# Performance work log

Hardware: AMD Instinct MI355X
Metric: run time of the kernel (lower is better)

The kernel has to match this reference:

```python
import jax, jax.numpy as jnp
import numpy as np

B, S, H = 8, 1024, 1024
NH, HD = 16, 64
LN_EPS = 1e-12


def setup_inputs() -> dict:
    key = jax.random.key(0)
    ks = jax.random.split(key, 8)
    sd = 0.02
    return {
        "hidden_states": jax.random.normal(ks[0], (B, S, H), jnp.float32),
        "attention_mask": jnp.zeros((B, 1, 1, S), jnp.float32),
        "Wq": jax.random.normal(ks[1], (H, H), jnp.float32) * sd,
        "bq": jnp.zeros((H,), jnp.float32),
        "Wk": jax.random.normal(ks[2], (H, H), jnp.float32) * sd,
        "bk": jnp.zeros((H,), jnp.float32),
        "Wv": jax.random.normal(ks[3], (H, H), jnp.float32) * sd,
        "bv": jnp.zeros((H,), jnp.float32),
        "Wo": jax.random.normal(ks[4], (H, H), jnp.float32) * sd,
        "bo": jnp.zeros((H,), jnp.float32),
        "ln_gamma": jnp.ones((H,), jnp.float32),
        "ln_beta": jnp.zeros((H,), jnp.float32),
    }


def _heads(x):
    # [B,S,H] -> [B,NH,S,HD]
    return x.reshape(B, S, NH, HD).transpose(0, 2, 1, 3)


def reference(hidden_states, attention_mask, Wq, bq, Wk, bk, Wv, bv, Wo, bo, ln_gamma, ln_beta):
    # QKV projections (torch Linear: x @ W.T + b)
    q = _heads(hidden_states @ Wq.T + bq)
    k = _heads(hidden_states @ Wk.T + bk)
    v = _heads(hidden_states @ Wv.T + bv)
    # scaled dot-product attention with additive mask
    scores = jnp.einsum("bhqd,bhkd->bhqk", q, k) / np.sqrt(HD).astype(np.float32)
    scores = scores + attention_mask  # broadcast [B,1,1,S]
    probs = jax.nn.softmax(scores, axis=-1)
    ctx = jnp.einsum("bhqk,bhkd->bhqd", probs, v)
    ctx = ctx.transpose(0, 2, 1, 3).reshape(B, S, H)
    # output projection + residual + LayerNorm
    out = ctx @ Wo.T + bo
    x = out + hidden_states
    mu = jnp.mean(x, axis=-1, keepdims=True)
    var = jnp.var(x, axis=-1, keepdims=True)
    return (x - mu) * jax.lax.rsqrt(var + LN_EPS) * ln_gamma + ln_beta
```

## Files before the change

kernel.cpp:

```cpp
#include <hip/hip_runtime.h>
#include <stdint.h>

typedef __attribute__((ext_vector_type(8))) __bf16 bf16x8;
typedef __attribute__((ext_vector_type(8))) unsigned short ushortx8;
typedef __attribute__((ext_vector_type(4))) unsigned short ushortx4;
typedef __attribute__((ext_vector_type(4))) short short4v;
typedef __attribute__((ext_vector_type(4))) float floatx4;

#define ASYNC16(g, l) __builtin_amdgcn_global_load_lds( \
    (__attribute__((address_space(1))) void*)(g),       \
    (__attribute__((address_space(3))) void*)(l), 16, 0, 0)

__device__ __forceinline__ unsigned short f2bf(float f) {
    unsigned int u = __float_as_uint(f);
    u += 0x7fffu + ((u >> 16) & 1u);
    return (unsigned short)(u >> 16);
}

__device__ __forceinline__ floatx4 mfma32(bf16x8 a, bf16x8 b, floatx4 c) {
    return __builtin_amdgcn_mfma_f32_16x16x32_bf16(a, b, c, 0, 0, 0);
}
__device__ __forceinline__ floatx4 mfma16(short4v a, short4v b, floatx4 c) {
    return __builtin_amdgcn_mfma_f32_16x16x16bf16_1k(a, b, c, 0, 0, 0);
}

__global__ __launch_bounds__(256) void cvt_bf16(const float* __restrict__ in,
                                                unsigned short* __restrict__ out,
                                                int n8) {
    int i = blockIdx.x * 256 + threadIdx.x;
    if (i >= n8) return;
    const float4* p = (const float4*)in + (size_t)i * 2;
    float4 a = p[0], b = p[1];
    ushortx8 o;
    o[0] = f2bf(a.x); o[1] = f2bf(a.y); o[2] = f2bf(a.z); o[3] = f2bf(a.w);
    o[4] = f2bf(b.x); o[5] = f2bf(b.y); o[6] = f2bf(b.z); o[7] = f2bf(b.w);
    *((ushortx8*)out + i) = o;
}

__global__ __launch_bounds__(256) void gemm_qkv(
    const unsigned short* __restrict__ A,
    const unsigned short* __restrict__ W,
    const float* __restrict__ bq, const float* __restrict__ bk, const float* __restrict__ bv,
    unsigned short* __restrict__ Qo, unsigned short* __restrict__ Ko, unsigned short* __restrict__ Vo)
{
    __shared__ unsigned short As[128 * 32];
    __shared__ unsigned short Bs[128 * 32];
    const int K = 1024;
    const int t = threadIdx.x;
    const int wave = t >> 6, lane = t & 63;
    const int quad = lane >> 4, l16 = lane & 15;
    const int wm = (wave >> 1) * 64, wn = (wave & 1) * 64;

    const unsigned short* Ag = A + (size_t)blockIdx.x * 128 * K + (t >> 2) * K + (t & 3) * 8;
    const unsigned short* Wg = W + (size_t)blockIdx.y * 128 * K + (t >> 2) * K + (t & 3) * 8;

    floatx4 acc[4][4] = {};

    for (int k0 = 0; k0 < K; k0 += 32) {
        __syncthreads();
        ASYNC16(Ag + k0,          As + t * 8);
        ASYNC16(Ag + 64 * K + k0, As + 2048 + t * 8);
        ASYNC16(Wg + k0,          Bs + t * 8);
        ASYNC16(Wg + 64 * K + k0, Bs + 2048 + t * 8);
        __syncthreads();
        bf16x8 af[4], bfr[4];
#pragma unroll
        for (int mt = 0; mt < 4; mt++)
            af[mt] = *(const bf16x8*)(As + (wm + mt * 16 + l16) * 32 + quad * 8);
#pragma unroll
        for (int nt = 0; nt < 4; nt++)
            bfr[nt] = *(const bf16x8*)(Bs + (wn + nt * 16 + l16) * 32 + quad * 8);
#pragma unroll
        for (int mt = 0; mt < 4; mt++)
#pragma unroll
            for (int nt = 0; nt < 4; nt++)
                acc[mt][nt] = mfma32(af[mt], bfr[nt], acc[mt][nt]);
    }

    int mat = (blockIdx.y * 128) >> 10;
    if (mat == 2) {
#pragma unroll
        for (int nt = 0; nt < 4; nt++) {
            int feat = (blockIdx.y * 128 + wn + nt * 16 + l16) & 1023;
            float bias = bv[feat];
            int h = feat >> 6, d = feat & 63;
#pragma unroll
            for (int mt = 0; mt < 4; mt++) {
                int sg = blockIdx.x * 128 + wm + mt * 16 + quad * 4;
                int b = sg >> 10, s = sg & 1023;
                ushortx4 o4;
#pragma unroll
                for (int r = 0; r < 4; r++) o4[r] = f2bf(acc[mt][nt][r] + bias);
                *(ushortx4*)(Vo + (((size_t)(b * 16 + h) * 64 + d) * 1024 + s)) = o4;
            }
        }
    } else {
        const float* bp = (mat == 0) ? bq : bk;
        unsigned short* op = (mat == 0) ? Qo : Ko;
#pragma unroll
        for (int nt = 0; nt < 4; nt++) {
            int feat = (blockIdx.y * 128 + wn + nt * 16 + l16) & 1023;
            float bias = bp[feat];
            int h = feat >> 6, d = feat & 63;
#pragma unroll
            for (int mt = 0; mt < 4; mt++) {
#pragma unroll
                for (int r = 0; r < 4; r++) {
                    int gm = blockIdx.x * 128 + wm + mt * 16 + quad * 4 + r;
                    int b = gm >> 10, s = gm & 1023;
                    op[(((size_t)b * 16 + h) * 1024 + s) * 64 + d] = f2bf(acc[mt][nt][r] + bias);
                }
            }
        }
    }
}

__global__ __launch_bounds__(256) void attn(
    const unsigned short* __restrict__ Q,
    const unsigned short* __restrict__ Kg,
    const unsigned short* __restrict__ Vt,
    const float* __restrict__ mask,
    unsigned short* __restrict__ ctx)
{
    __shared__ unsigned short Qs[64 * 64];
    __shared__ unsigned short Ks[64 * 64];
    __shared__ unsigned short Vs[64 * 64];
    __shared__ float Msall[1024];

    const int t = threadIdx.x;
    const int wave = t >> 6, lane = t & 63, quad = lane >> 4, l16 = lane & 15;
    const int s7 = l16 & 7;
    const int head = blockIdx.y;
    const int b = head >> 4, h = head & 15;
    const int q0 = blockIdx.x * 64;
    const unsigned short* Qh = Q + (size_t)head * 65536;
    const unsigned short* Kh = Kg + (size_t)head * 65536;
    const unsigned short* Vh = Vt + (size_t)head * 65536;

    *(float4*)(Msall + t * 4) = *(const float4*)(mask + b * 1024 + t * 4);

    {
        int row = t >> 3, cg = (t & 7) ^ (row & 7);
        ASYNC16(Qh + (size_t)(q0 + row) * 64 + cg * 8, Qs + t * 8);
        ASYNC16(Qh + (size_t)(q0 + row + 32) * 64 + cg * 8, Qs + 2048 + t * 8);
    }
    __syncthreads();
    int qrow = wave * 16 + l16;
    bf16x8 qf0 = *(const bf16x8*)(Qs + qrow * 64 + ((quad ^ s7) * 8));
    bf16x8 qf1 = *(const bf16x8*)(Qs + qrow * 64 + (((quad + 4) ^ s7) * 8));

    float rs_acc = 0.f;
    floatx4 o_acc[4] = {};

    for (int k0 = 0; k0 < 1024; k0 += 64) {
        __syncthreads();
        {
            int row = t >> 3, cg = (t & 7) ^ (row & 7);
            ASYNC16(Kh + (size_t)(k0 + row) * 64 + cg * 8, Ks + t * 8);
            ASYNC16(Kh + (size_t)(k0 + row + 32) * 64 + cg * 8, Ks + 2048 + t * 8);
            ASYNC16(Vh + (size_t)row * 1024 + k0 + cg * 8, Vs + t * 8);
            ASYNC16(Vh + (size_t)(row + 32) * 1024 + k0 + cg * 8, Vs + 2048 + t * 8);
        }
        __syncthreads();

        floatx4 st[4];
#pragma unroll
        for (int nt = 0; nt < 4; nt++) {
            int krow = nt * 16 + l16;
            bf16x8 kf0 = *(const bf16x8*)(Ks + krow * 64 + ((quad ^ s7) * 8));
            bf16x8 kf1 = *(const bf16x8*)(Ks + krow * 64 + (((quad + 4) ^ s7) * 8));
            floatx4 z = {0.f, 0.f, 0.f, 0.f};
            z = mfma32(kf0, qf0, z);
            st[nt] = mfma32(kf1, qf1, z);
        }

        short4v pf[4];
#pragma unroll
        for (int nt = 0; nt < 4; nt++) {
            floatx4 mk = *(const floatx4*)(Msall + k0 + nt * 16 + quad * 4);
#pragma unroll
            for (int r = 0; r < 4; r++) {
                float p = __expf(st[nt][r] * 0.125f + mk[r]);
                rs_acc += p;
                pf[nt][r] = (short)(__float_as_uint(p) >> 16);
            }
        }

#pragma unroll
        for (int dt = 0; dt < 4; dt++) {
            int vrow = dt * 16 + l16;
#pragma unroll
            for (int nt = 0; nt < 4; nt++) {
                short4v vf = *(const short4v*)(Vs + vrow * 64 +
                                (((2 * nt + (quad >> 1)) ^ s7) * 8) + (quad & 1) * 4);
                o_acc[dt] = mfma16(vf, pf[nt], o_acc[dt]);
            }
        }
    }

    rs_acc += __shfl_xor(rs_acc, 16);
    rs_acc += __shfl_xor(rs_acc, 32);
    float inv_l = 1.0f / rs_acc;

    int qg = q0 + wave * 16 + l16;
#pragma unroll
    for (int dt = 0; dt < 4; dt++) {
        ushortx4 o4;
#pragma unroll
        for (int r = 0; r < 4; r++) o4[r] = f2bf(o_acc[dt][r] * inv_l);
        *(ushortx4*)(ctx + ((size_t)(b * 1024 + qg)) * 1024 + h * 64 + dt * 16 + quad * 4) = o4;
    }
}

__global__ __launch_bounds__(256) void gemm_proj(
    const unsigned short* __restrict__ A,
    const unsigned short* __restrict__ W,
    const float* __restrict__ bo,
    const float* __restrict__ resid,
    float* __restrict__ X)
{
    __shared__ unsigned short As[128 * 32];
    __shared__ unsigned short Bs[128 * 32];
    const int K = 1024;
    const int t = threadIdx.x;
    const int wave = t >> 6, lane = t & 63;
    const int quad = lane >> 4, l16 = lane & 15;
    const int wm = (wave >> 1) * 64, wn = (wave & 1) * 64;

    const unsigned short* Ag = A + (size_t)blockIdx.x * 128 * K + (t >> 2) * K + (t & 3) * 8;
    const unsigned short* Wg = W + (size_t)blockIdx.y * 128 * K + (t >> 2) * K + (t & 3) * 8;

    floatx4 acc[4][4] = {};

    for (int k0 = 0; k0 < K; k0 += 32) {
        __syncthreads();
        ASYNC16(Ag + k0,          As + t * 8);
        ASYNC16(Ag + 64 * K + k0, As + 2048 + t * 8);
        ASYNC16(Wg + k0,          Bs + t * 8);
        ASYNC16(Wg + 64 * K + k0, Bs + 2048 + t * 8);
        __syncthreads();
        bf16x8 af[4], bfr[4];
#pragma unroll
        for (int mt = 0; mt < 4; mt++)
            af[mt] = *(const bf16x8*)(As + (wm + mt * 16 + l16) * 32 + quad * 8);
#pragma unroll
        for (int nt = 0; nt < 4; nt++)
            bfr[nt] = *(const bf16x8*)(Bs + (wn + nt * 16 + l16) * 32 + quad * 8);
#pragma unroll
        for (int mt = 0; mt < 4; mt++)
#pragma unroll
            for (int nt = 0; nt < 4; nt++)
                acc[mt][nt] = mfma32(af[mt], bfr[nt], acc[mt][nt]);
    }

#pragma unroll
    for (int nt = 0; nt < 4; nt++) {
        int gn = blockIdx.y * 128 + wn + nt * 16 + l16;
        float bias = bo[gn];
#pragma unroll
        for (int mt = 0; mt < 4; mt++) {
#pragma unroll
            for (int r = 0; r < 4; r++) {
                int gm = blockIdx.x * 128 + wm + mt * 16 + quad * 4 + r;
                size_t off = (size_t)gm * 1024 + gn;
                X[off] = acc[mt][nt][r] + bias + resid[off];
            }
        }
    }
}

__global__ __launch_bounds__(256) void ln_k(const float* __restrict__ X,
                                            const float* __restrict__ g,
                                            const float* __restrict__ be,
                                            float* __restrict__ out)
{
    int row = blockIdx.x;
    int t = threadIdx.x;
    const float* xr = X + (size_t)row * 1024;
    float4 v = *(const float4*)(xr + t * 4);
    float s = v.x + v.y + v.z + v.w;
    float ss = v.x * v.x + v.y * v.y + v.z * v.z + v.w * v.w;
    for (int off = 1; off < 64; off <<= 1) {
        s += __shfl_xor(s, off);
        ss += __shfl_xor(ss, off);
    }
    __shared__ float red[8];
    int wave = t >> 6, lane = t & 63;
    if (lane == 0) { red[wave] = s; red[4 + wave] = ss; }
    __syncthreads();
    s = red[0] + red[1] + red[2] + red[3];
    ss = red[4] + red[5] + red[6] + red[7];
    float mu = s * (1.f / 1024.f);
    float var = ss * (1.f / 1024.f) - mu * mu;
    float inv = rsqrtf(var + 1e-12f);
    float4 gv = *(const float4*)(g + t * 4);
    float4 bv = *(const float4*)(be + t * 4);
    float4 o;
    o.x = (v.x - mu) * inv * gv.x + bv.x;
    o.y = (v.y - mu) * inv * gv.y + bv.y;
    o.z = (v.z - mu) * inv * gv.z + bv.z;
    o.w = (v.w - mu) * inv * gv.w + bv.w;
    *(float4*)(out + (size_t)row * 1024 + t * 4) = o;
}

extern "C" void kernel_launch(void* const* d_in, const int* in_sizes, int n_in,
                              void* d_out, int out_size, void* d_ws, size_t ws_size,
                              hipStream_t stream)
{
    const float* hidden = (const float*)d_in[0];
    const float* mask   = (const float*)d_in[1];
    const float* Wq = (const float*)d_in[2];
    const float* bq = (const float*)d_in[3];
    const float* Wk = (const float*)d_in[4];
    const float* bk = (const float*)d_in[5];
    const float* Wv = (const float*)d_in[6];
    const float* bv = (const float*)d_in[7];
    const float* Wo = (const float*)d_in[8];
    const float* bo = (const float*)d_in[9];
    const float* gamma = (const float*)d_in[10];
    const float* beta  = (const float*)d_in[11];
    float* out = (float*)d_out;

    char* ws = (char*)d_ws;
    unsigned short* hid_bf  = (unsigned short*)(ws + 0);
    unsigned short* wqkv_bf = (unsigned short*)(ws + 16777216);
    unsigned short* wo_bf   = (unsigned short*)(ws + 23068672);
    unsigned short* vt_bf   = (unsigned short*)(ws + 25165824);
    unsigned short* ctx_bf  = (unsigned short*)(ws + 41943040);
    unsigned short* q_bf    = (unsigned short*)(ws + 58720256);
    unsigned short* k_bf    = (unsigned short*)(ws + 75497472);
    float* x_f = (float*)(ws + 58720256);

    cvt_bf16<<<4096, 256, 0, stream>>>(hidden, hid_bf, 1048576);
    cvt_bf16<<<512, 256, 0, stream>>>(Wq, wqkv_bf, 131072);
    cvt_bf16<<<512, 256, 0, stream>>>(Wk, wqkv_bf + 1048576, 131072);
    cvt_bf16<<<512, 256, 0, stream>>>(Wv, wqkv_bf + 2097152, 131072);
    cvt_bf16<<<512, 256, 0, stream>>>(Wo, wo_bf, 131072);

    gemm_qkv<<<dim3(64, 24), 256, 0, stream>>>(hid_bf, wqkv_bf, bq, bk, bv, q_bf, k_bf, vt_bf);
    attn<<<dim3(16, 128), 256, 0, stream>>>(q_bf, k_bf, vt_bf, mask, ctx_bf);
    gemm_proj<<<dim3(64, 8), 256, 0, stream>>>(ctx_bf, wo_bf, bo, hidden, x_f);
    ln_k<<<8192, 256, 0, stream>>>(x_f, gamma, beta, out);
}
```

Baseline: 302.1 us.

## Swizzle GEMM LDS tiles, vectorize Q/K stores via swapped MFMA, merge weight casts

Applies an XOR swizzle to the LDS staging column in all GEMMs to cut bank conflicts on fragment reads. It splits the QKV GEMM into separate Q/K and V kernels. The Q/K kernel swaps the MFMA operand order so each lane holds four consecutive features and can write 8-byte vector stores with float4 bias loads, instead of scalar 2-byte scattered stores. It also merges the four weight-conversion launches into one kernel, trading an extra GEMM launch for fewer launches overall.

```diff
diff --git a/kernel.cpp b/kernel.cpp
--- a/kernel.cpp
+++ b/kernel.cpp
@@ -37,25 +37,34 @@
     *((ushortx8*)out + i) = o;
 }
 
-__global__ __launch_bounds__(256) void gemm_qkv(
-    const unsigned short* __restrict__ A,
-    const unsigned short* __restrict__ W,
-    const float* __restrict__ bq, const float* __restrict__ bk, const float* __restrict__ bv,
-    unsigned short* __restrict__ Qo, unsigned short* __restrict__ Ko, unsigned short* __restrict__ Vo)
-{
-    __shared__ unsigned short As[128 * 32];
-    __shared__ unsigned short Bs[128 * 32];
+__global__ __launch_bounds__(256) void cvt_w(const float* __restrict__ Wq,
+                                             const float* __restrict__ Wk,
+                                             const float* __restrict__ Wv,
+                                             const float* __restrict__ Wo,
+                                             unsigned short* __restrict__ oqkv,
+                                             unsigned short* __restrict__ oo) {
+    int blk = blockIdx.x >> 9;
+    const float* src = (blk == 0) ? Wq : (blk == 1) ? Wk : (blk == 2) ? Wv : Wo;
+    unsigned short* dst = (blk == 3) ? oo : oqkv + (size_t)blk * 1048576;
+    int i = (blockIdx.x & 511) * 256 + threadIdx.x;
+    const float4* p = (const float4*)src + (size_t)i * 2;
+    float4 a = p[0], b = p[1];
+    ushortx8 o;
+    o[0] = f2bf(a.x); o[1] = f2bf(a.y); o[2] = f2bf(a.z); o[3] = f2bf(a.w);
+    o[4] = f2bf(b.x); o[5] = f2bf(b.y); o[6] = f2bf(b.z); o[7] = f2bf(b.w);
+    *((ushortx8*)dst + i) = o;
+}
+
+template<bool SWAP>
+__device__ __forceinline__ void kloop_128(
+    const unsigned short* __restrict__ Ag,
+    const unsigned short* __restrict__ Wg,
+    unsigned short* As, unsigned short* Bs,
+    int wm, int wn, int l16, int quad, int t,
+    floatx4 acc[4][4])
+{
     const int K = 1024;
-    const int t = threadIdx.x;
-    const int wave = t >> 6, lane = t & 63;
-    const int quad = lane >> 4, l16 = lane & 15;
-    const int wm = (wave >> 1) * 64, wn = (wave & 1) * 64;
-
-    const unsigned short* Ag = A + (size_t)blockIdx.x * 128 * K + (t >> 2) * K + (t & 3) * 8;
-    const unsigned short* Wg = W + (size_t)blockIdx.y * 128 * K + (t >> 2) * K + (t & 3) * 8;
-
-    floatx4 acc[4][4] = {};
-
+#pragma unroll 1
     for (int k0 = 0; k0 < K; k0 += 32) {
         __syncthreads();
         ASYNC16(Ag + k0,          As + t * 8);
@@ -65,52 +74,109 @@
         __syncthreads();
         bf16x8 af[4], bfr[4];
 #pragma unroll
-        for (int mt = 0; mt < 4; mt++)
-            af[mt] = *(const bf16x8*)(As + (wm + mt * 16 + l16) * 32 + quad * 8);
-#pragma unroll
-        for (int nt = 0; nt < 4; nt++)
-            bfr[nt] = *(const bf16x8*)(Bs + (wn + nt * 16 + l16) * 32 + quad * 8);
-#pragma unroll
-        for (int mt = 0; mt < 4; mt++)
-#pragma unroll
-            for (int nt = 0; nt < 4; nt++)
-                acc[mt][nt] = mfma32(af[mt], bfr[nt], acc[mt][nt]);
-    }
-
-    int mat = (blockIdx.y * 128) >> 10;
-    if (mat == 2) {
+        for (int mt = 0; mt < 4; mt++) {
+            int row = wm + mt * 16 + l16;
+            int p = quad ^ ((row >> 1) & 3);
+            af[mt] = *(const bf16x8*)(As + row * 32 + p * 8);
+        }
 #pragma unroll
         for (int nt = 0; nt < 4; nt++) {
-            int feat = (blockIdx.y * 128 + wn + nt * 16 + l16) & 1023;
-            float bias = bv[feat];
-            int h = feat >> 6, d = feat & 63;
-#pragma unroll
-            for (int mt = 0; mt < 4; mt++) {
-                int sg = blockIdx.x * 128 + wm + mt * 16 + quad * 4;
-                int b = sg >> 10, s = sg & 1023;
-                ushortx4 o4;
-#pragma unroll
-                for (int r = 0; r < 4; r++) o4[r] = f2bf(acc[mt][nt][r] + bias);
-                *(ushortx4*)(Vo + (((size_t)(b * 16 + h) * 64 + d) * 1024 + s)) = o4;
-            }
-        }
-    } else {
-        const float* bp = (mat == 0) ? bq : bk;
-        unsigned short* op = (mat == 0) ? Qo : Ko;
-#pragma unroll
-        for (int nt = 0; nt < 4; nt++) {
-            int feat = (blockIdx.y * 128 + wn + nt * 16 + l16) & 1023;
-            float bias = bp[feat];
-            int h = feat >> 6, d = feat & 63;
-#pragma unroll
-            for (int mt = 0; mt < 4; mt++) {
-#pragma unroll
-                for (int r = 0; r < 4; r++) {
-                    int gm = blockIdx.x * 128 + wm + mt * 16 + quad * 4 + r;
-                    int b = gm >> 10, s = gm & 1023;
-                    op[(((size_t)b * 16 + h) * 1024 + s) * 64 + d] = f2bf(acc[mt][nt][r] + bias);
-                }
-            }
+            int row = wn + nt * 16 + l16;
+            int p = quad ^ ((row >> 1) & 3);
+            bfr[nt] = *(const bf16x8*)(Bs + row * 32 + p * 8);
+        }
+        if (SWAP) {
+#pragma unroll
+            for (int ft = 0; ft < 4; ft++)
+#pragma unroll
+                for (int st = 0; st < 4; st++)
+                    acc[ft][st] = mfma32(bfr[ft], af[st], acc[ft][st]);
+        } else {
+#pragma unroll
+            for (int mt = 0; mt < 4; mt++)
+#pragma unroll
+                for (int nt = 0; nt < 4; nt++)
+                    acc[mt][nt] = mfma32(af[mt], bfr[nt], acc[mt][nt]);
+        }
+    }
+}
+
+__device__ __forceinline__ int stage_col(int t) { return ((t & 3) ^ ((t >> 3) & 3)) * 8; }
+
+__global__ __launch_bounds__(256) void gemm_qk(
+    const unsigned short* __restrict__ A,
+    const unsigned short* __restrict__ W,
+    const float* __restrict__ bq, const float* __restrict__ bk,
+    unsigned short* __restrict__ Qo, unsigned short* __restrict__ Ko)
+{
+    __shared__ unsigned short As[128 * 32];
+    __shared__ unsigned short Bs[128 * 32];
+    const int K = 1024;
+    const int t = threadIdx.x;
+    const int wave = t >> 6, lane = t & 63;
+    const int quad = lane >> 4, l16 = lane & 15;
+    const int wm = (wave >> 1) * 64, wn = (wave & 1) * 64;
+
+    const unsigned short* Ag = A + (size_t)blockIdx.x * 128 * K + (t >> 2) * K + stage_col(t);
+    const unsigned short* Wg = W + (size_t)blockIdx.y * 128 * K + (t >> 2) * K + stage_col(t);
+
+    floatx4 acc[4][4] = {};
+    kloop_128<true>(Ag, Wg, As, Bs, wm, wn, l16, quad, t, acc);
+
+    const float* bp = (blockIdx.y < 8) ? bq : bk;
+    unsigned short* op = (blockIdx.y < 8) ? Qo : Ko;
+#pragma unroll
+    for (int ft = 0; ft < 4; ft++) {
+        int featg = (blockIdx.y * 128 + wn + ft * 16 + quad * 4) & 1023;
+        float4 b4 = *(const float4*)(bp + featg);
+        int h = featg >> 6, d = featg & 63;
+#pragma unroll
+        for (int st = 0; st < 4; st++) {
+            int sg = blockIdx.x * 128 + wm + st * 16 + l16;
+            int b = sg >> 10, s = sg & 1023;
+            ushortx4 o4;
+            o4[0] = f2bf(acc[ft][st][0] + b4.x);
+            o4[1] = f2bf(acc[ft][st][1] + b4.y);
+            o4[2] = f2bf(acc[ft][st][2] + b4.z);
+            o4[3] = f2bf(acc[ft][st][3] + b4.w);
+            *(ushortx4*)(op + (((size_t)(b * 16 + h) * 1024 + s) * 64 + d)) = o4;
+        }
+    }
+}
+
+__global__ __launch_bounds__(256) void gemm_v(
+    const unsigned short* __restrict__ A,
+    const unsigned short* __restrict__ W,
+    const float* __restrict__ bv,
+    unsigned short* __restrict__ Vo)
+{
+    __shared__ unsigned short As[128 * 32];
+    __shared__ unsigned short Bs[128 * 32];
+    const int K = 1024;
+    const int t = threadIdx.x;
+    const int wave = t >> 6, lane = t & 63;
+    const int quad = lane >> 4, l16 = lane & 15;
+    const int wm = (wave >> 1) * 64, wn = (wave & 1) * 64;
+
+    const unsigned short* Ag = A + (size_t)blockIdx.x * 128 * K + (t >> 2) * K + stage_col(t);
+    const unsigned short* Wg = W + (size_t)blockIdx.y * 128 * K + (t >> 2) * K + stage_col(t);
+
+    floatx4 acc[4][4] = {};
+    kloop_128<false>(Ag, Wg, As, Bs, wm, wn, l16, quad, t, acc);
+
+#pragma unroll
+    for (int nt = 0; nt < 4; nt++) {
+        int feat = (blockIdx.y * 128 + wn + nt * 16 + l16) & 1023;
+        float bias = bv[feat];
+        int h = feat >> 6, d = feat & 63;
+#pragma unroll
+        for (int mt = 0; mt < 4; mt++) {
+            int sg = blockIdx.x * 128 + wm + mt * 16 + quad * 4;
+            int b = sg >> 10, s = sg & 1023;
+            ushortx4 o4;
+#pragma unroll
+            for (int r = 0; r < 4; r++) o4[r] = f2bf(acc[mt][nt][r] + bias);
+            *(ushortx4*)(Vo + (((size_t)(b * 16 + h) * 64 + d) * 1024 + s)) = o4;
         }
     }
 }
@@ -227,31 +293,11 @@
     const int quad = lane >> 4, l16 = lane & 15;
     const int wm = (wave >> 1) * 64, wn = (wave & 1) * 64;
 
-    const unsigned short* Ag = A + (size_t)blockIdx.x * 128 * K + (t >> 2) * K + (t & 3) * 8;
-    const unsigned short* Wg = W + (size_t)blockIdx.y * 128 * K + (t >> 2) * K + (t & 3) * 8;
+    const unsigned short* Ag = A + (size_t)blockIdx.x * 128 * K + (t >> 2) * K + stage_col(t);
+    const unsigned short* Wg = W + (size_t)blockIdx.y * 128 * K + (t >> 2) * K + stage_col(t);
 
     floatx4 acc[4][4] = {};
-
-    for (int k0 = 0; k0 < K; k0 += 32) {
-        __syncthreads();
-        ASYNC16(Ag + k0,          As + t * 8);
-        ASYNC16(Ag + 64 * K + k0, As + 2048 + t * 8);
-        ASYNC16(Wg + k0,          Bs + t * 8);
-        ASYNC16(Wg + 64 * K + k0, Bs + 2048 + t * 8);
-        __syncthreads();
-        bf16x8 af[4], bfr[4];
-#pragma unroll
-        for (int mt = 0; mt < 4; mt++)
-            af[mt] = *(const bf16x8*)(As + (wm + mt * 16 + l16) * 32 + quad * 8);
-#pragma unroll
-        for (int nt = 0; nt < 4; nt++)
-            bfr[nt] = *(const bf16x8*)(Bs + (wn + nt * 16 + l16) * 32 + quad * 8);
-#pragma unroll
-        for (int mt = 0; mt < 4; mt++)
-#pragma unroll
-            for (int nt = 0; nt < 4; nt++)
-                acc[mt][nt] = mfma32(af[mt], bfr[nt], acc[mt][nt]);
-    }
+    kloop_128<false>(Ag, Wg, As, Bs, wm, wn, l16, quad, t, acc);
 
 #pragma unroll
     for (int nt = 0; nt < 4; nt++) {
@@ -332,12 +378,10 @@
     float* x_f = (float*)(ws + 58720256);
 
     cvt_bf16<<<4096, 256, 0, stream>>>(hidden, hid_bf, 1048576);
-    cvt_bf16<<<512, 256, 0, stream>>>(Wq, wqkv_bf, 131072);
-    cvt_bf16<<<512, 256, 0, stream>>>(Wk, wqkv_bf + 1048576, 131072);
-    cvt_bf16<<<512, 256, 0, stream>>>(Wv, wqkv_bf + 2097152, 131072);
-    cvt_bf16<<<512, 256, 0, stream>>>(Wo, wo_bf, 131072);
-
-    gemm_qkv<<<dim3(64, 24), 256, 0, stream>>>(hid_bf, wqkv_bf, bq, bk, bv, q_bf, k_bf, vt_bf);
+    cvt_w<<<2048, 256, 0, stream>>>(Wq, Wk, Wv, Wo, wqkv_bf, wo_bf);
+
+    gemm_qk<<<dim3(64, 16), 256, 0, stream>>>(hid_bf, wqkv_bf, bq, bk, q_bf, k_bf);
+    gemm_v<<<dim3(64, 8), 256, 0, stream>>>(hid_bf, wqkv_bf + 2097152, bv, vt_bf);
     attn<<<dim3(16, 128), 256, 0, stream>>>(q_bf, k_bf, vt_bf, mask, ctx_bf);
     gemm_proj<<<dim3(64, 8), 256, 0, stream>>>(ctx_bf, wo_bf, bo, hidden, x_f);
     ln_k<<<8192, 256, 0, stream>>>(x_f, gamma, beta, out);
```

Measured after the change: 308.9 us. 2.2% more time.
